# Kernel tuning notes

Measured on AMD Instinct MI355X. Metric: run time of the kernel, lower is better.

Reference implementation:

```python
import jax, jax.numpy as jnp
import numpy as np

B, S, H = 1, 2048, 4096
NH = 32
NOPE, ROPE, VD = 128, 64, 128
QHD = NOPE + ROPE          # 192
QLR, KVLR = 1536, 512
BASE = 10000.0
EPS = 1e-6
SCALE = QHD ** -0.5


def _rmsnorm(x, w):
    xf = x.astype(jnp.float32)
    var = jnp.mean(xf * xf, axis=-1, keepdims=True)
    return (w * (xf * jax.lax.rsqrt(var + EPS))).astype(x.dtype)


def _rope_tables(seq_len):
    inv_freq = 1.0 / (BASE ** (jnp.arange(0, ROPE, 2, dtype=jnp.float32) / ROPE))
    t = jnp.arange(seq_len, dtype=jnp.float32)
    freqs = jnp.outer(t, inv_freq)                     # [S, ROPE/2]
    emb = jnp.concatenate([freqs, freqs], axis=-1)     # [S, ROPE]
    return jnp.cos(emb), jnp.sin(emb)


def _rotate_half(x):
    d = x.shape[-1] // 2
    return jnp.concatenate([-x[..., d:], x[..., :d]], axis=-1)


def setup_inputs() -> dict:
    key = jax.random.key(0)
    ks = jax.random.split(key, 8)
    w = 0.02
    hidden_states = jax.random.normal(ks[0], (B, S, H), dtype=jnp.float32)
    # additive causal mask, 0 on/below diagonal, -1e9 above
    causal = jnp.tril(jnp.ones((S, S), dtype=bool))
    attention_mask = jnp.where(causal, 0.0, -1e9).astype(jnp.float32)[None, None]
    return {
        "hidden_states": hidden_states,
        "attention_mask": attention_mask,
        "Wqa": jax.random.normal(ks[1], (QLR, H), dtype=jnp.float32) * w,
        "qa_ln_w": jnp.ones((QLR,), dtype=jnp.float32),
        "Wqb": jax.random.normal(ks[2], (NH * QHD, QLR), dtype=jnp.float32) * w,
        "Wkva": jax.random.normal(ks[3], (KVLR + ROPE, H), dtype=jnp.float32) * w,
        "kva_ln_w": jnp.ones((KVLR,), dtype=jnp.float32),
        "Wkvb": jax.random.normal(ks[4], (NH * (NOPE + VD), KVLR), dtype=jnp.float32) * w,
        "Wo": jax.random.normal(ks[5], (H, NH * VD), dtype=jnp.float32) * w,
    }


def reference(hidden_states, attention_mask, Wqa, qa_ln_w, Wqb, Wkva, kva_ln_w, Wkvb, Wo):
    bsz, q_len, _ = hidden_states.shape
    # --- Q path: low-rank down-proj + RMSNorm + up-proj ---
    q = _rmsnorm(hidden_states @ Wqa.T, qa_ln_w) @ Wqb.T          # [B,S,NH*QHD]
    q = q.reshape(bsz, q_len, NH, QHD).transpose(0, 2, 1, 3)      # [B,NH,S,QHD]
    q_nope, q_pe = q[..., :NOPE], q[..., NOPE:]
    # --- KV path: shared low-rank compression + decoupled rope key ---
    ckv = hidden_states @ Wkva.T                                   # [B,S,KVLR+ROPE]
    compressed_kv, k_pe = ckv[..., :KVLR], ckv[..., KVLR:]
    k_pe = k_pe.reshape(bsz, q_len, 1, ROPE).transpose(0, 2, 1, 3)  # [B,1,S,ROPE]
    kv = _rmsnorm(compressed_kv, kva_ln_w) @ Wkvb.T                # [B,S,NH*(NOPE+VD)]
    kv = kv.reshape(bsz, q_len, NH, NOPE + VD).transpose(0, 2, 1, 3)
    k_nope, value_states = kv[..., :NOPE], kv[..., NOPE:]
    # --- RoPE on decoupled dims ---
    cos, sin = _rope_tables(q_len)                                 # [S,ROPE] broadcast over B,NH
    q_pe = q_pe * cos + _rotate_half(q_pe) * sin
    k_pe = k_pe * cos + _rotate_half(k_pe) * sin
    query_states = jnp.concatenate([q_nope, q_pe], axis=-1)        # [B,NH,S,QHD]
    key_states = jnp.concatenate(
        [k_nope, jnp.broadcast_to(k_pe, (bsz, NH, q_len, ROPE))], axis=-1)
    # --- SDPA ---
    attn = jnp.einsum('bhqd,bhkd->bhqk', query_states, key_states) * SCALE
    attn = attn + attention_mask
    attn = jax.nn.softmax(attn.astype(jnp.float32), axis=-1).astype(query_states.dtype)
    out = jnp.einsum('bhqk,bhkd->bhqd', attn, value_states)        # [B,NH,S,VD]
    out = out.transpose(0, 2, 1, 3).reshape(bsz, q_len, NH * VD)
    return out @ Wo.T
```

## Files before the change

kernel.cpp:

```cpp
#include <hip/hip_runtime.h>

typedef __bf16 bf16;
typedef __bf16 bf16x8 __attribute__((ext_vector_type(8)));
typedef __bf16 bf16x4 __attribute__((ext_vector_type(4)));
typedef float  f32x4  __attribute__((ext_vector_type(4)));

#define NH_    32
#define S_     2048
#define H_     4096
#define NOPE_  128
#define ROPE_  64
#define VD_    128
#define QHD_   192
#define QLR_   1536
#define KVLR_  512
#define QKVA_N 2176

#define MFMA16(a, b, c) __builtin_amdgcn_mfma_f32_16x16x32_bf16(a, b, c, 0, 0, 0)

__device__ __forceinline__ void async_lds16(void* lds, const void* g) {
  __builtin_amdgcn_global_load_lds(
      (const __attribute__((address_space(1))) void*)g,
      (__attribute__((address_space(3))) void*)lds,
      16, 0, 0);
}

#define CVN1 2097152LL
#define CVN2 1572864LL
#define CVN3 655360LL
#define CVN4 2359296LL
#define CVN5 1048576LL
#define CVN6 4194304LL
#define CVN7 16384LL
#define CVC1 (CVN1)
#define CVC2 (CVC1 + CVN2)
#define CVC3 (CVC2 + CVN3)
#define CVC4 (CVC3 + CVN4)
#define CVC5 (CVC4 + CVN5)
#define CVC6 (CVC5 + CVN6)
#define CVC7 (CVC6 + CVN7)

__device__ __forceinline__ void cv4(const float* __restrict__ s, bf16* __restrict__ d,
                                    long long i) {
  float4 v = ((const float4*)s)[i];
  bf16x4 o;
  o[0] = (bf16)v.x; o[1] = (bf16)v.y; o[2] = (bf16)v.z; o[3] = (bf16)v.w;
  ((bf16x4*)d)[i] = o;
}

__global__ __launch_bounds__(256) void convert_all_kernel(
    const float* __restrict__ hs, const float* __restrict__ Wqa,
    const float* __restrict__ Wkva, const float* __restrict__ Wqb,
    const float* __restrict__ Wkvb, const float* __restrict__ Wo,
    bf16* __restrict__ hidden_bf, bf16* __restrict__ qkva_w,
    bf16* __restrict__ Wqb_bf, bf16* __restrict__ Wkvb_bf,
    bf16* __restrict__ Wo_bf, float* __restrict__ ct, float* __restrict__ st) {
  long long i = (long long)blockIdx.x * 256 + threadIdx.x;
  const long long stride = (long long)gridDim.x * 256;
  for (; i < CVC7; i += stride) {
    if (i < CVC1) {
      cv4(hs, hidden_bf, i);
    } else if (i < CVC2) {
      cv4(Wqa, qkva_w, i - CVC1);
    } else if (i < CVC3) {
      long long j = i - CVC2;
      long long r = j >> 10;
      bf16x4 o;
      if (r < 576) {
        float4 v = ((const float4*)Wkva)[j];
        o[0] = (bf16)v.x; o[1] = (bf16)v.y; o[2] = (bf16)v.z; o[3] = (bf16)v.w;
      } else {
        o[0] = o[1] = o[2] = o[3] = (bf16)0.f;
      }
      ((bf16x4*)(qkva_w + (size_t)QLR_ * H_))[j] = o;
    } else if (i < CVC4) {
      cv4(Wqb, Wqb_bf, i - CVC3);
    } else if (i < CVC5) {
      cv4(Wkvb, Wkvb_bf, i - CVC4);
    } else if (i < CVC6) {
      cv4(Wo, Wo_bf, i - CVC5);
    } else {
      long long j4 = (i - CVC6) * 4;
#pragma unroll
      for (int k = 0; k < 4; ++k) {
        long long idx = j4 + k;
        int t = (int)(idx >> 5), f = (int)(idx & 31);
        float inv = powf(10000.0f, -(float)f / 32.0f);
        float ang = (float)t * inv;
        ct[idx] = cosf(ang);
        st[idx] = sinf(ang);
      }
    }
  }
}

__global__ __launch_bounds__(256) void norm_rope_kernel(
    const float* __restrict__ part, const float* __restrict__ qa_ln,
    const float* __restrict__ kva_ln, bf16* __restrict__ qa_norm,
    bf16* __restrict__ ckv_norm, bf16* __restrict__ kpe,
    const float* __restrict__ ct, const float* __restrict__ st, long long pstr) {
  const int row = blockIdx.x;
  const int tid = threadIdx.x;
  const float* xr = part + (size_t)row * QKVA_N;
  float ssq = 0.f, ssk = 0.f;
#pragma unroll
  for (int it = 0; it < 6; ++it) {
    float v = xr[tid + it * 256] + xr[tid + it * 256 + pstr];
    ssq += v * v;
  }
#pragma unroll
  for (int it = 6; it < 8; ++it) {
    float v = xr[tid + it * 256] + xr[tid + it * 256 + pstr];
    ssk += v * v;
  }
  __shared__ float redq[4], redk[4];
  for (int o = 32; o > 0; o >>= 1) {
    ssq += __shfl_down(ssq, o);
    ssk += __shfl_down(ssk, o);
  }
  if ((tid & 63) == 0) { redq[tid >> 6] = ssq; redk[tid >> 6] = ssk; }
  __syncthreads();
  float rq = 1.0f / sqrtf((redq[0] + redq[1] + redq[2] + redq[3]) / (float)QLR_ + 1e-6f);
  float rk = 1.0f / sqrtf((redk[0] + redk[1] + redk[2] + redk[3]) / (float)KVLR_ + 1e-6f);
#pragma unroll
  for (int it = 0; it < 6; ++it) {
    int i = tid + it * 256;
    float v = xr[i] + xr[i + pstr];
    qa_norm[(size_t)row * QLR_ + i] = (bf16)(qa_ln[i] * v * rq);
  }
#pragma unroll
  for (int it = 6; it < 8; ++it) {
    int i = tid + it * 256;
    float v = xr[i] + xr[i + pstr];
    ckv_norm[(size_t)row * KVLR_ + (i - 1536)] = (bf16)(kva_ln[i - 1536] * v * rk);
  }
  if (tid < 32) {
    int j = tid;
    float a = xr[2048 + j] + xr[2048 + j + pstr];
    float b = xr[2048 + 32 + j] + xr[2048 + 32 + j + pstr];
    float c = ct[row * 32 + j], s = st[row * 32 + j];
    kpe[row * 64 + j]      = (bf16)(a * c - b * s);
    kpe[row * 64 + 32 + j] = (bf16)(b * c + a * s);
  }
}

template <typename OutT, bool VOUT = false, int NSPLIT = 1, bool QROPE = false>
__global__ __launch_bounds__(256) void gemm_bt(const bf16* __restrict__ A,
                                               const bf16* __restrict__ B,
                                               OutT* __restrict__ C,
                                               bf16* __restrict__ vTout,
                                               const float* __restrict__ ct,
                                               const float* __restrict__ st,
                                               int M, int N, int K) {
  __shared__ bf16 SM[2 * 128 * 64];
  bf16* As = SM;
  bf16* Bs = SM + 128 * 64;
  const int tid = threadIdx.x;
  const int lane = tid & 63;
  const int w = tid >> 6;
  const int wm = w >> 1, wn = w & 1;

  const int nwg = gridDim.x * gridDim.y;
  const int lin = blockIdx.y * gridDim.x + blockIdx.x;
  const int cpx = nwg >> 3;
  const int swz = (lin & 7) * cpx + (lin >> 3);
  const int bx = swz % gridDim.x, by = swz / gridDim.x;

  const int m0 = by * 128, n0 = bx * 128;
  const int r15 = lane & 15;
  const int kbase = (lane >> 4) * 8;

  const int klen = K / NSPLIT;
  const int koff = (NSPLIT > 1) ? (int)blockIdx.z * klen : 0;
  OutT* Cz = (NSPLIT > 1) ? C + (size_t)blockIdx.z * M * (size_t)N : C;

  f32x4 acc[4][4];
#pragma unroll
  for (int i = 0; i < 4; ++i)
#pragma unroll
    for (int j = 0; j < 4; ++j) acc[i][j] = (f32x4){0.f, 0.f, 0.f, 0.f};

  for (int k0 = koff; k0 < koff + klen; k0 += 64) {
    __syncthreads();
#pragma unroll
    for (int s = 0; s < 4; ++s) {
      int lrow = w * 32 + s * 8 + (lane >> 3);
      int sc = (lane & 7) ^ (lrow & 7);
      const bf16* ga = A + (size_t)(m0 + lrow) * K + k0 + sc * 8;
      const bf16* gb = B + (size_t)(n0 + lrow) * K + k0 + sc * 8;
      async_lds16((char*)As + w * 4096 + s * 1024, ga);
      async_lds16((char*)Bs + w * 4096 + s * 1024, gb);
    }
    __syncthreads();

#pragma unroll
    for (int kk = 0; kk < 2; ++kk) {
      bf16x8 af[4], bfr[4];
#pragma unroll
      for (int i = 0; i < 4; ++i) {
        int ar = wm * 64 + i * 16 + r15;
        int off = ar * 128 + (kk * 32 + kbase) * 2;
        off ^= (ar & 7) << 4;
        af[i] = *(const bf16x8*)((const char*)As + off);
      }
#pragma unroll
      for (int j = 0; j < 4; ++j) {
        int br = wn * 64 + j * 16 + r15;
        int off = br * 128 + (kk * 32 + kbase) * 2;
        off ^= (br & 7) << 4;
        bfr[j] = *(const bf16x8*)((const char*)Bs + off);
      }
#pragma unroll
      for (int i = 0; i < 4; ++i)
#pragma unroll
        for (int j = 0; j < 4; ++j)
          acc[i][j] = MFMA16(af[i], bfr[j], acc[i][j]);
    }
  }

  const int rq = lane >> 4;

  if constexpr (VOUT) {
    if (bx & 1) {
      const int hh = bx >> 1;
      __syncthreads();
      bf16* TB = SM;
#pragma unroll
      for (int i = 0; i < 4; ++i)
#pragma unroll
        for (int j = 0; j < 4; ++j) {
          int cl = wn * 64 + j * 16 + r15;
          int rw0 = wm * 64 + i * 16 + rq * 4;
          bf16x4 hv;
#pragma unroll
          for (int r = 0; r < 4; ++r) hv[r] = (bf16)acc[i][j][r];
          *(bf16x4*)&TB[cl * 128 + (rw0 ^ ((cl & 7) << 3))] = hv;
        }
      __syncthreads();
#pragma unroll
      for (int it = 0; it < 8; ++it) {
        int cid = tid + it * 256;
        int dd = cid >> 4, cc = cid & 15;
        bf16x8 v = *(const bf16x8*)&TB[dd * 128 + ((cc ^ (dd & 7)) * 8)];
        *(bf16x8*)(vTout + ((size_t)hh * 128 + dd) * (size_t)M + m0 + cc * 8) = v;
      }
      return;
    }
  }

  if constexpr (QROPE) {
    if (((bx << 1) + wn) % 3 == 2) {
#pragma unroll
      for (int i = 0; i < 4; ++i)
#pragma unroll
        for (int r = 0; r < 4; ++r) {
          int t = m0 + wm * 64 + i * 16 + rq * 4 + r;
#pragma unroll
          for (int jf = 0; jf < 2; ++jf) {
            int j = jf * 16 + r15;
            float c = ct[t * 32 + j], s = st[t * 32 + j];
            float a = acc[i][jf][r], b = acc[i][jf + 2][r];
            acc[i][jf][r]     = a * c - b * s;
            acc[i][jf + 2][r] = b * c + a * s;
          }
        }
    }
  }

#pragma unroll
  for (int i = 0; i < 4; ++i)
#pragma unroll
    for (int j = 0; j < 4; ++j)
#pragma unroll
      for (int r = 0; r < 4; ++r) {
        int row = m0 + wm * 64 + i * 16 + rq * 4 + r;
        int col = n0 + wn * 64 + j * 16 + r15;
        Cz[(size_t)row * N + col] = (OutT)acc[i][j][r];
      }
}

__global__ __launch_bounds__(256) void attn_fwd(const bf16* __restrict__ q,
                                                const bf16* __restrict__ kv,
                                                const bf16* __restrict__ vT,
                                                const bf16* __restrict__ kpe,
                                                bf16* __restrict__ out) {
  __shared__ bf16 KN[64][136];
  __shared__ bf16 KP[64][72];
  __shared__ bf16 VS[128 * 64];
  __shared__ bf16 PS[4][16][72];

  const int h = blockIdx.x;
  const int qt = (gridDim.y - 1) - blockIdx.y;
  const int q0 = qt * 64;
  const int tid = threadIdx.x;
  const int lane = tid & 63;
  const int w = tid >> 6;
  const int r15 = lane & 15;
  const int g = lane >> 4;
  const int kbase = g * 8;

  const float SCALE = 0.07216878364870322f;
  const float CS = SCALE * 1.4426950408889634f;
  const float RTH = 8.0f / SCALE;

  bf16x8 qf[6];
  {
    const size_t qrow = q0 + w * 16 + r15;
    const bf16* qp = q + qrow * (NH_ * QHD_) + h * QHD_;
#pragma unroll
    for (int c = 0; c < 6; ++c) qf[c] = *(const bf16x8*)(qp + c * 32 + kbase);
  }

  f32x4 o[9];
#pragma unroll
  for (int d = 0; d < 9; ++d) o[d] = (f32x4){0.f, 0.f, 0.f, 0.f};
  float m[4] = {-1e30f, -1e30f, -1e30f, -1e30f};
  bf16x8 vone;
#pragma unroll
  for (int j = 0; j < 8; ++j) vone[j] = (bf16)1.f;

  const int pr_r = tid >> 4, pr_c = tid & 15;
  const int kp_r = tid >> 2, kp_c = tid & 3;
  const int vd = w * 32 + (lane >> 3);
  const int vc = lane & 7;
  const int vp = vc ^ (vd & 7);
  bf16x8 pKN[4], pV[4], pKP[2];
  auto load_tile = [&](int k0) {
#pragma unroll
    for (int it = 0; it < 4; ++it) {
      pKN[it] = *(const bf16x8*)(kv + (size_t)(k0 + pr_r + it * 16) * (NH_ * 256) + h * 256 + pr_c * 8);
      pV[it]  = *(const bf16x8*)(vT + ((size_t)h * 128 + vd + it * 8) * (size_t)S_ + k0 + vc * 8);
    }
    pKP[0] = *(const bf16x8*)(kpe + (size_t)(k0 + kp_r) * 64 + kp_c * 16);
    pKP[1] = *(const bf16x8*)(kpe + (size_t)(k0 + kp_r) * 64 + kp_c * 16 + 8);
  };

  load_tile(0);

  for (int kt = 0; kt <= qt; ++kt) {
    const int k0 = kt * 64;
    __syncthreads();
#pragma unroll
    for (int it = 0; it < 4; ++it) {
      *(bf16x8*)&KN[pr_r + it * 16][pr_c * 8] = pKN[it];
      *(bf16x8*)((char*)VS + (vd + it * 8) * 128 + vp * 16) = pV[it];
    }
    *(bf16x8*)&KP[kp_r][kp_c * 16] = pKP[0];
    *(bf16x8*)&KP[kp_r][kp_c * 16 + 8] = pKP[1];
    __syncthreads();

    if (kt < qt) load_tile(k0 + 64);

    f32x4 s[4];
    __builtin_amdgcn_s_setprio(1);
#pragma unroll
    for (int ct = 0; ct < 4; ++ct) {
      f32x4 a = (f32x4){0.f, 0.f, 0.f, 0.f};
#pragma unroll
      for (int c = 0; c < 4; ++c) {
        bf16x8 b = *(const bf16x8*)&KN[ct * 16 + r15][c * 32 + kbase];
        a = MFMA16(qf[c], b, a);
      }
#pragma unroll
      for (int c = 0; c < 2; ++c) {
        bf16x8 b = *(const bf16x8*)&KP[ct * 16 + r15][c * 32 + kbase];
        a = MFMA16(qf[4 + c], b, a);
      }
      s[ct] = a;
    }
    __builtin_amdgcn_s_setprio(0);

    const int qrow0 = q0 + w * 16 + g * 4;
    if (kt == qt) {
#pragma unroll
      for (int ct = 0; ct < 4; ++ct)
#pragma unroll
        for (int r = 0; r < 4; ++r)
          if ((k0 + ct * 16 + r15) > (qrow0 + r)) s[ct][r] = -1e30f;
    }

    float lm[4];
#pragma unroll
    for (int r = 0; r < 4; ++r)
      lm[r] = fmaxf(fmaxf(s[0][r], s[1][r]), fmaxf(s[2][r], s[3][r]));
    bool over = (lm[0] > m[0] + RTH) || (lm[1] > m[1] + RTH) ||
                (lm[2] > m[2] + RTH) || (lm[3] > m[3] + RTH);
    if (__any(over)) {
#pragma unroll
      for (int r = 0; r < 4; ++r) {
        float v = lm[r];
        v = fmaxf(v, __shfl_xor(v, 1));
        v = fmaxf(v, __shfl_xor(v, 2));
        v = fmaxf(v, __shfl_xor(v, 4));
        v = fmaxf(v, __shfl_xor(v, 8));
        float mn = fmaxf(m[r], v);
        float sc = exp2f((m[r] - mn) * CS);
        m[r] = mn;
#pragma unroll
        for (int d = 0; d < 9; ++d) o[d][r] *= sc;
      }
    }
#pragma unroll
    for (int ct = 0; ct < 4; ++ct)
#pragma unroll
      for (int r = 0; r < 4; ++r)
        PS[w][g * 4 + r][ct * 16 + r15] = (bf16)exp2f((s[ct][r] - m[r]) * CS);

    __builtin_amdgcn_s_setprio(1);
#pragma unroll
    for (int kk = 0; kk < 2; ++kk) {
      bf16x8 pa = *(const bf16x8*)&PS[w][r15][kk * 32 + kbase];
      const int kcx = (kk * 4 + g) ^ (r15 & 7);
      o[8] = MFMA16(pa, vone, o[8]);
#pragma unroll
      for (int dt = 0; dt < 8; ++dt) {
        int d = dt * 16 + r15;
        bf16x8 vb = *(const bf16x8*)((const char*)VS + d * 128 + kcx * 16);
        o[dt] = MFMA16(pa, vb, o[dt]);
      }
    }
    __builtin_amdgcn_s_setprio(0);
  }

  float invl[4];
#pragma unroll
  for (int r = 0; r < 4; ++r) invl[r] = 1.0f / o[8][r];
#pragma unroll
  for (int dt = 0; dt < 8; ++dt)
#pragma unroll
    for (int r = 0; r < 4; ++r) {
      int row = q0 + w * 16 + g * 4 + r;
      out[(size_t)row * (NH_ * VD_) + h * VD_ + dt * 16 + r15] = (bf16)(o[dt][r] * invl[r]);
    }
}

extern "C" void kernel_launch(void* const* d_in, const int* in_sizes, int n_in,
                              void* d_out, int out_size, void* d_ws, size_t ws_size,
                              hipStream_t stream) {
  (void)in_sizes; (void)n_in; (void)out_size; (void)ws_size;
  const float* hs     = (const float*)d_in[0];
  const float* Wqa    = (const float*)d_in[2];
  const float* qa_ln  = (const float*)d_in[3];
  const float* Wqb    = (const float*)d_in[4];
  const float* Wkva   = (const float*)d_in[5];
  const float* kva_ln = (const float*)d_in[6];
  const float* Wkvb   = (const float*)d_in[7];
  const float* Wo     = (const float*)d_in[8];
  float* outp = (float*)d_out;

  char* W = (char*)d_ws;
  size_t off = 0;
  auto nxt = [&](size_t b) { size_t o = off; off += (b + 255) & ~(size_t)255; return o; };
  bf16*  hidden_bf = (bf16*)(W + nxt((size_t)S_ * H_ * 2));
  bf16*  qkva_w    = (bf16*)(W + nxt((size_t)QKVA_N * H_ * 2));
  bf16*  Wqb_bf    = (bf16*)(W + nxt((size_t)NH_ * QHD_ * QLR_ * 2));
  bf16*  Wkvb_bf   = (bf16*)(W + nxt((size_t)NH_ * 256 * KVLR_ * 2));
  bf16*  Wo_bf     = (bf16*)(W + nxt((size_t)H_ * NH_ * VD_ * 2));
  bf16*  qa_norm   = (bf16*)(W + nxt((size_t)S_ * QLR_ * 2));
  bf16*  ckv_norm  = (bf16*)(W + nxt((size_t)S_ * KVLR_ * 2));
  bf16*  kpe       = (bf16*)(W + nxt((size_t)S_ * ROPE_ * 2));
  float* cost      = (float*)(W + nxt((size_t)S_ * 32 * 4));
  float* sint      = (float*)(W + nxt((size_t)S_ * 32 * 4));
  size_t Roff = nxt((size_t)S_ * NH_ * QHD_ * 2 + (size_t)S_ * NH_ * 256 * 2 +
                    (size_t)NH_ * VD_ * S_ * 2 + (size_t)S_ * NH_ * VD_ * 2);
  bf16* q_bf     = (bf16*)(W + Roff);
  bf16* kv_bf    = (bf16*)(W + Roff + (size_t)S_ * NH_ * QHD_ * 2);
  bf16* vT       = (bf16*)(W + Roff + (size_t)S_ * NH_ * QHD_ * 2 + (size_t)S_ * NH_ * 256 * 2);
  bf16* attn_out = (bf16*)(W + Roff + (size_t)S_ * NH_ * QHD_ * 2 + (size_t)S_ * NH_ * 256 * 2 +
                           (size_t)NH_ * VD_ * S_ * 2);
  float* part    = (float*)(W + Roff);
  const long long PSTR = (long long)S_ * QKVA_N;

  convert_all_kernel<<<2048, 256, 0, stream>>>(hs, Wqa, Wkva, Wqb, Wkvb, Wo,
                                               hidden_bf, qkva_w, Wqb_bf, Wkvb_bf, Wo_bf,
                                               cost, sint);

  gemm_bt<float, false, 2><<<dim3(QKVA_N / 128, S_ / 128, 2), 256, 0, stream>>>(
      hidden_bf, qkva_w, part, nullptr, nullptr, nullptr, S_, QKVA_N, H_);

  norm_rope_kernel<<<S_, 256, 0, stream>>>(part, qa_ln, kva_ln, qa_norm, ckv_norm,
                                           kpe, cost, sint, PSTR);

  gemm_bt<bf16, false, 1, true><<<dim3(NH_ * QHD_ / 128, S_ / 128), 256, 0, stream>>>(
      qa_norm, Wqb_bf, q_bf, nullptr, cost, sint, S_, NH_ * QHD_, QLR_);

  gemm_bt<bf16, true><<<dim3(NH_ * 256 / 128, S_ / 128), 256, 0, stream>>>(
      ckv_norm, Wkvb_bf, kv_bf, vT, nullptr, nullptr, S_, NH_ * 256, KVLR_);

  attn_fwd<<<dim3(NH_, S_ / 64), 256, 0, stream>>>(q_bf, kv_bf, vT, kpe, attn_out);

  gemm_bt<float><<<dim3(H_ / 128, S_ / 128), 256, 0, stream>>>(
      attn_out, Wo_bf, outp, nullptr, nullptr, nullptr, S_, H_, H_);
}
```

Measured before the change: 396.2 us.

## Split Q RoPE into separate kernel and remap GEMM tile order

Moves the RoPE rotation of the query's positional part out of the Q up-projection GEMM epilogue into a standalone elementwise kernel that rewrites q in place. It also changes the swizzled block-to-tile mapping in every GEMM so consecutive workgroups walk along M (rows) instead of N. The mapping change targets L2 reuse of the weight tiles. The separate RoPE kernel adds an extra launch plus a read and write of the rope part of q, but makes the GEMM template simpler.

```diff
diff --git a/kernel.cpp b/kernel.cpp
--- a/kernel.cpp
+++ b/kernel.cpp
@@ -94,6 +94,20 @@
   }
 }
 
+__global__ __launch_bounds__(256) void rope_q_kernel(bf16* __restrict__ qb,
+                                                     const float* __restrict__ ct,
+                                                     const float* __restrict__ st) {
+  int i = blockIdx.x * 256 + threadIdx.x;
+  int t = i >> 10;
+  int rem = i & 1023;
+  int h = rem >> 5, j = rem & 31;
+  size_t base = (size_t)t * (NH_ * QHD_) + h * QHD_ + NOPE_;
+  float a = (float)qb[base + j], b = (float)qb[base + 32 + j];
+  float c = ct[t * 32 + j], s = st[t * 32 + j];
+  qb[base + j]      = (bf16)(a * c - b * s);
+  qb[base + 32 + j] = (bf16)(b * c + a * s);
+}
+
 __global__ __launch_bounds__(256) void norm_rope_kernel(
     const float* __restrict__ part, const float* __restrict__ qa_ln,
     const float* __restrict__ kva_ln, bf16* __restrict__ qa_norm,
@@ -144,13 +158,11 @@
   }
 }
 
-template <typename OutT, bool VOUT = false, int NSPLIT = 1, bool QROPE = false>
+template <typename OutT, bool VOUT = false, int NSPLIT = 1>
 __global__ __launch_bounds__(256) void gemm_bt(const bf16* __restrict__ A,
                                                const bf16* __restrict__ B,
                                                OutT* __restrict__ C,
                                                bf16* __restrict__ vTout,
-                                               const float* __restrict__ ct,
-                                               const float* __restrict__ st,
                                                int M, int N, int K) {
   __shared__ bf16 SM[2 * 128 * 64];
   bf16* As = SM;
@@ -164,7 +176,7 @@
   const int lin = blockIdx.y * gridDim.x + blockIdx.x;
   const int cpx = nwg >> 3;
   const int swz = (lin & 7) * cpx + (lin >> 3);
-  const int bx = swz % gridDim.x, by = swz / gridDim.x;
+  const int by = swz % gridDim.y, bx = swz / gridDim.y;
 
   const int m0 = by * 128, n0 = bx * 128;
   const int r15 = lane & 15;
@@ -245,25 +257,6 @@
         *(bf16x8*)(vTout + ((size_t)hh * 128 + dd) * (size_t)M + m0 + cc * 8) = v;
       }
       return;
-    }
-  }
-
-  if constexpr (QROPE) {
-    if (((bx << 1) + wn) % 3 == 2) {
-#pragma unroll
-      for (int i = 0; i < 4; ++i)
-#pragma unroll
-        for (int r = 0; r < 4; ++r) {
-          int t = m0 + wm * 64 + i * 16 + rq * 4 + r;
-#pragma unroll
-          for (int jf = 0; jf < 2; ++jf) {
-            int j = jf * 16 + r15;
-            float c = ct[t * 32 + j], s = st[t * 32 + j];
-            float a = acc[i][jf][r], b = acc[i][jf + 2][r];
-            acc[i][jf][r]     = a * c - b * s;
-            acc[i][jf + 2][r] = b * c + a * s;
-          }
-        }
     }
   }
 
@@ -476,19 +469,20 @@
                                                cost, sint);
 
   gemm_bt<float, false, 2><<<dim3(QKVA_N / 128, S_ / 128, 2), 256, 0, stream>>>(
-      hidden_bf, qkva_w, part, nullptr, nullptr, nullptr, S_, QKVA_N, H_);
+      hidden_bf, qkva_w, part, nullptr, S_, QKVA_N, H_);
 
   norm_rope_kernel<<<S_, 256, 0, stream>>>(part, qa_ln, kva_ln, qa_norm, ckv_norm,
                                            kpe, cost, sint, PSTR);
 
-  gemm_bt<bf16, false, 1, true><<<dim3(NH_ * QHD_ / 128, S_ / 128), 256, 0, stream>>>(
-      qa_norm, Wqb_bf, q_bf, nullptr, cost, sint, S_, NH_ * QHD_, QLR_);
+  gemm_bt<bf16><<<dim3(NH_ * QHD_ / 128, S_ / 128), 256, 0, stream>>>(
+      qa_norm, Wqb_bf, q_bf, nullptr, S_, NH_ * QHD_, QLR_);
+  rope_q_kernel<<<8192, 256, 0, stream>>>(q_bf, cost, sint);
 
   gemm_bt<bf16, true><<<dim3(NH_ * 256 / 128, S_ / 128), 256, 0, stream>>>(
-      ckv_norm, Wkvb_bf, kv_bf, vT, nullptr, nullptr, S_, NH_ * 256, KVLR_);
+      ckv_norm, Wkvb_bf, kv_bf, vT, S_, NH_ * 256, KVLR_);
 
   attn_fwd<<<dim3(NH_, S_ / 64), 256, 0, stream>>>(q_bf, kv_bf, vT, kpe, attn_out);
 
   gemm_bt<float><<<dim3(H_ / 128, S_ / 128), 256, 0, stream>>>(
-      attn_out, Wo_bf, outp, nullptr, nullptr, nullptr, S_, H_, H_);
-}
+      attn_out, Wo_bf, outp, nullptr, S_, H_, H_);
+}
```

Measured after the change: 414.1 us. 1.05x slower.
